# Kernel tuning notes

Hardware: AMD Instinct MI355X
Metric: run time of the kernel (lower is better)

The kernel has to match this reference:

```python
import jax, jax.numpy as jnp
import numpy as np

NUM_NODES = 10000   # nodes per graph (softmax axis)
N_HEADS = 8
IN_CHANNELS = 32
NUM_GRAPHS = 64
TOTAL_NODES = NUM_NODES * NUM_GRAPHS


def setup_inputs() -> dict:
    key = jax.random.key(0)
    k_x, k_b, k_att = jax.random.split(key, 3)
    x = jax.random.normal(k_x, (TOTAL_NODES, IN_CHANNELS), dtype=jnp.float32)
    batch = jnp.sort(jax.random.randint(k_b, (TOTAL_NODES,), 0, NUM_GRAPHS)).astype(jnp.int64)
    att = jax.random.normal(k_att, (N_HEADS, NUM_NODES), dtype=jnp.float32)
    return {"x": x, "batch": batch, "att": att, "num_graphs": NUM_GRAPHS}


def reference(x, batch, att, num_graphs):
    # x: [N, C], batch: [N], att: [H, M]; N == M * num_graphs
    B = int(num_graphs)
    w = jax.nn.softmax(att, axis=1)          # [H, M] softmax over per-graph node slots
    w_full = jnp.tile(w, (1, B))             # [H, N] tiled per graph (repeat(1,B).view(-1,1))
    # per-head weighted scatter-add pooling keyed by batch id
    pooled = jax.vmap(
        lambda wh: jax.ops.segment_sum(x * wh[:, None], batch, num_segments=B)
    )(w_full)                                # [H, B, C]
    # torch.cat(pools, dim=-1): head-major blocks along feature axis
    return pooled.transpose(1, 0, 2).reshape(B, -1)  # [B, H*C]
```

## Files before the change

### kernel.cpp

```cpp
#include <hip/hip_runtime.h>
#include <math.h>

#define H 8
#define C 32
#define HC 256
#define KSL 32
#define PB 16

__device__ __forceinline__ float wred_sum(float v) {
#pragma unroll
    for (int o = 32; o; o >>= 1) v += __shfl_xor(v, o, 64);
    return v;
}
__device__ __forceinline__ float4 red4_no(float4 v) {
#pragma unroll
    for (int o = 8; o < 64; o <<= 1) {
        v.x += __shfl_xor(v.x, o, 64);
        v.y += __shfl_xor(v.y, o, 64);
        v.z += __shfl_xor(v.z, o, 64);
        v.w += __shfl_xor(v.w, o, 64);
    }
    return v;
}

__global__ __launch_bounds__(256) void prep_kernel(
        const float* __restrict__ att, const int* __restrict__ batch,
        float* __restrict__ wtabT, int* __restrict__ segend,
        float* __restrict__ partials, int M, int Ntot, int tb, int sb) {
    const int bid = blockIdx.x;
    if (bid < tb) {
        const int idx = bid * 256 + threadIdx.x;
        if (idx < H * M) {
            const int hh = idx & (H - 1);
            const int mm = idx >> 3;
            wtabT[idx] = __expf(att[(size_t)hh * M + mm]);
        }
    } else if (bid < tb + sb) {
        const int idx = (bid - tb) * 256 + threadIdx.x;
        if (idx < Ntot) {
            const int b = batch[idx];
            if (idx == Ntot - 1 || batch[idx + 1] != b) segend[b] = idx + 1;
        }
    } else {
        const int pbid = bid - tb - sb;
        const int h = pbid / PB;
        const int p = pbid % PB;
        const int s0 = (int)(((long)M * p) / PB);
        const int s1 = (int)(((long)M * (p + 1)) / PB);
        const float* __restrict__ row = att + (size_t)h * M;
        __shared__ float red[4];
        float s = 0.f;
        for (int i = s0 + threadIdx.x; i < s1; i += 256) s += __expf(row[i]);
        s = wred_sum(s);
        if ((threadIdx.x & 63) == 0) red[threadIdx.x >> 6] = s;
        __syncthreads();
        if (threadIdx.x == 0)
            partials[h * PB + p] = red[0] + red[1] + red[2] + red[3];
    }
}

#define FMA8(XV, W0, W1)                                              \
    a0.x = fmaf(XV.x, W0.x, a0.x); a0.y = fmaf(XV.y, W0.x, a0.y);     \
    a0.z = fmaf(XV.z, W0.x, a0.z); a0.w = fmaf(XV.w, W0.x, a0.w);     \
    a1.x = fmaf(XV.x, W0.y, a1.x); a1.y = fmaf(XV.y, W0.y, a1.y);     \
    a1.z = fmaf(XV.z, W0.y, a1.z); a1.w = fmaf(XV.w, W0.y, a1.w);     \
    a2.x = fmaf(XV.x, W0.z, a2.x); a2.y = fmaf(XV.y, W0.z, a2.y);     \
    a2.z = fmaf(XV.z, W0.z, a2.z); a2.w = fmaf(XV.w, W0.z, a2.w);     \
    a3.x = fmaf(XV.x, W0.w, a3.x); a3.y = fmaf(XV.y, W0.w, a3.y);     \
    a3.z = fmaf(XV.z, W0.w, a3.z); a3.w = fmaf(XV.w, W0.w, a3.w);     \
    a4.x = fmaf(XV.x, W1.x, a4.x); a4.y = fmaf(XV.y, W1.x, a4.y);     \
    a4.z = fmaf(XV.z, W1.x, a4.z); a4.w = fmaf(XV.w, W1.x, a4.w);     \
    a5.x = fmaf(XV.x, W1.y, a5.x); a5.y = fmaf(XV.y, W1.y, a5.y);     \
    a5.z = fmaf(XV.z, W1.y, a5.z); a5.w = fmaf(XV.w, W1.y, a5.w);     \
    a6.x = fmaf(XV.x, W1.z, a6.x); a6.y = fmaf(XV.y, W1.z, a6.y);     \
    a6.z = fmaf(XV.z, W1.z, a6.z); a6.w = fmaf(XV.w, W1.z, a6.w);     \
    a7.x = fmaf(XV.x, W1.w, a7.x); a7.y = fmaf(XV.y, W1.w, a7.y);     \
    a7.z = fmaf(XV.z, W1.w, a7.z); a7.w = fmaf(XV.w, W1.w, a7.w);

__global__ __launch_bounds__(256, 5) void poolA_kernel(
        const float* __restrict__ x, const float* __restrict__ wtabT,
        const int* __restrict__ segend, float* __restrict__ psum,
        int M, int Ntot) {
    const int g  = blockIdx.x >> 5;
    const int k  = blockIdx.x & (KSL - 1);
    const int wv = threadIdx.x >> 6;
    const int lane = threadIdx.x & 63;
    const int cg = lane & 7;
    const int no = lane >> 3;
    const int c  = cg << 2;

    const int s0 = (g == 0) ? 0 : segend[g - 1];
    const int s1 = segend[g];
    const int L  = s1 - s0;
    const int sb = s0 + (int)(((long)L * k) >> 5);
    const int sl = (s0 + (int)(((long)L * (k + 1)) >> 5)) - sb;
    int       n    = sb + (sl * wv) / 4;
    const int nEnd = sb + (sl * (wv + 1)) / 4;

    float4 a0 = {0,0,0,0}, a1 = {0,0,0,0}, a2 = {0,0,0,0}, a3 = {0,0,0,0};
    float4 a4 = {0,0,0,0}, a5 = {0,0,0,0}, a6 = {0,0,0,0}, a7 = {0,0,0,0};

    int m = n % M;
    while (n < nEnd) {
        const int run = min(nEnd - n, M - m);
        const float* xb = x + (size_t)(n + no) * C + c;
        const float* wb = wtabT + ((size_t)(m + no) << 3);
        const int full = run & ~7;
        int i = 0;
#pragma unroll 2
        for (; i < full; i += 8) {
            const float4 xv  = *(const float4*)(xb + (size_t)i * C);
            const float4 wv0 = *(const float4*)(wb + (size_t)i * 8);
            const float4 wv1 = *(const float4*)(wb + (size_t)i * 8 + 4);
            FMA8(xv, wv0, wv1)
        }
        const int rem = run - full;
        if (rem) {
            const int off = (no < rem) ? no : 0;
            const float4 xv = *(const float4*)(x + (size_t)(n + i + off) * C + c);
            float4 wv0 = {0,0,0,0}, wv1 = {0,0,0,0};
            if (no < rem) {
                const float* wb2 = wtabT + ((size_t)(m + i + no) << 3);
                wv0 = *(const float4*)(wb2);
                wv1 = *(const float4*)(wb2 + 4);
            }
            FMA8(xv, wv0, wv1)
        }
        n += run;
        m += run;
        if (m >= M) m = 0;
    }

    a0 = red4_no(a0); a1 = red4_no(a1); a2 = red4_no(a2); a3 = red4_no(a3);
    a4 = red4_no(a4); a5 = red4_no(a5); a6 = red4_no(a6); a7 = red4_no(a7);

    __shared__ float4 sacc[4][H][8];
    if (no == 0) {
        sacc[wv][0][cg] = a0; sacc[wv][1][cg] = a1;
        sacc[wv][2][cg] = a2; sacc[wv][3][cg] = a3;
        sacc[wv][4][cg] = a4; sacc[wv][5][cg] = a5;
        sacc[wv][6][cg] = a6; sacc[wv][7][cg] = a7;
    }
    __syncthreads();
    if (wv == 0) {
        const int hh = lane >> 3;
        const int cc = lane & 7;
        float4 s  = sacc[0][hh][cc];
        float4 t1 = sacc[1][hh][cc];
        float4 t2 = sacc[2][hh][cc];
        float4 t3 = sacc[3][hh][cc];
        s.x += t1.x + t2.x + t3.x;
        s.y += t1.y + t2.y + t3.y;
        s.z += t1.z + t2.z + t3.z;
        s.w += t1.w + t2.w + t3.w;
        float* o = psum + ((size_t)blockIdx.x << 8) + (hh << 5) + (cc << 2);
        *(float4*)o = s;
    }
}

__global__ __launch_bounds__(256) void reduceB_kernel(
        const float* __restrict__ psum, const float* __restrict__ partials,
        float* __restrict__ out) {
    __shared__ float sinv[H];
    if (threadIdx.x < H) {
        float s = 0.f;
#pragma unroll
        for (int k = 0; k < PB; ++k) s += partials[threadIdx.x * PB + k];
        sinv[threadIdx.x] = 1.0f / s;
    }
    __syncthreads();
    const int g = blockIdx.x;
    const int i = threadIdx.x;
    const float* p = psum + ((size_t)g << 13) + i;
    float s = 0.f;
#pragma unroll
    for (int k = 0; k < KSL; ++k) s += p[(size_t)k << 8];
    out[(g << 8) + i] = s * sinv[i >> 5];
}

extern "C" void kernel_launch(void* const* d_in, const int* in_sizes, int n_in,
                              void* d_out, int out_size, void* d_ws, size_t ws_size,
                              hipStream_t stream) {
    const float* x     = (const float*)d_in[0];
    const int*   batch = (const int*)d_in[1];
    const float* att   = (const float*)d_in[2];
    float*       out   = (float*)d_out;

    const int Ntot = in_sizes[0] / C;
    const int M    = in_sizes[2] / H;
    const int B    = out_size / HC;

    float* partials = (float*)d_ws;
    int*   segend   = (int*)((char*)d_ws + 1024);
    float* wtabT    = (float*)((char*)d_ws + 4096);
    const size_t ps_off = (4096 + (size_t)H * M * sizeof(float) + 255) & ~(size_t)255;
    float* psum     = (float*)((char*)d_ws + ps_off);

    const int tb = (H * M + 255) / 256;
    const int sblocks = (Ntot + 255) / 256;
    prep_kernel<<<tb + sblocks + H * PB, 256, 0, stream>>>(
        att, batch, wtabT, segend, partials, M, Ntot, tb, sblocks);

    poolA_kernel<<<B * KSL, 256, 0, stream>>>(x, wtabT, segend, psum, M, Ntot);

    reduceB_kernel<<<B, 256, 0, stream>>>(psum, partials, out);
}
```

Baseline: 31.15 us.

## Fuse prep into pooling kernel with binary-search segments and on-the-fly exp weights

Removes the separate prep kernel. Segment boundaries are now found per block by binary search over the sorted batch array. Softmax numerators are computed inline with __expf from att using strided per-head loads instead of reading a precomputed transposed table. The softmax-denominator partial sums move into extra blocks of the pooling kernel. This saves a kernel launch and a workspace round trip, at the cost of 8 scattered loads plus 8 exps per node per lane and a log-depth search in every block.

```diff
diff --git a/kernel.cpp b/kernel.cpp
--- a/kernel.cpp
+++ b/kernel.cpp
@@ -22,41 +22,13 @@
     }
     return v;
 }
-
-__global__ __launch_bounds__(256) void prep_kernel(
-        const float* __restrict__ att, const int* __restrict__ batch,
-        float* __restrict__ wtabT, int* __restrict__ segend,
-        float* __restrict__ partials, int M, int Ntot, int tb, int sb) {
-    const int bid = blockIdx.x;
-    if (bid < tb) {
-        const int idx = bid * 256 + threadIdx.x;
-        if (idx < H * M) {
-            const int hh = idx & (H - 1);
-            const int mm = idx >> 3;
-            wtabT[idx] = __expf(att[(size_t)hh * M + mm]);
-        }
-    } else if (bid < tb + sb) {
-        const int idx = (bid - tb) * 256 + threadIdx.x;
-        if (idx < Ntot) {
-            const int b = batch[idx];
-            if (idx == Ntot - 1 || batch[idx + 1] != b) segend[b] = idx + 1;
-        }
-    } else {
-        const int pbid = bid - tb - sb;
-        const int h = pbid / PB;
-        const int p = pbid % PB;
-        const int s0 = (int)(((long)M * p) / PB);
-        const int s1 = (int)(((long)M * (p + 1)) / PB);
-        const float* __restrict__ row = att + (size_t)h * M;
-        __shared__ float red[4];
-        float s = 0.f;
-        for (int i = s0 + threadIdx.x; i < s1; i += 256) s += __expf(row[i]);
-        s = wred_sum(s);
-        if ((threadIdx.x & 63) == 0) red[threadIdx.x >> 6] = s;
-        __syncthreads();
-        if (threadIdx.x == 0)
-            partials[h * PB + p] = red[0] + red[1] + red[2] + red[3];
+__device__ __forceinline__ int lower_bound(const int* __restrict__ a, int n, int key) {
+    int lo = 0, hi = n;
+    while (lo < hi) {
+        const int mid = (lo + hi) >> 1;
+        if (a[mid] < key) lo = mid + 1; else hi = mid;
     }
+    return lo;
 }
 
 #define FMA8(XV, W0, W1)                                              \
@@ -77,20 +49,48 @@
     a7.x = fmaf(XV.x, W1.w, a7.x); a7.y = fmaf(XV.y, W1.w, a7.y);     \
     a7.z = fmaf(XV.z, W1.w, a7.z); a7.w = fmaf(XV.w, W1.w, a7.w);
 
+#define WLOAD8(MM, W0, W1)                                            \
+    { const float* ar = att + (MM);                                   \
+      W0.x = __expf(ar[0]);            W0.y = __expf(ar[M]);          \
+      W0.z = __expf(ar[2 * M]);        W0.w = __expf(ar[3 * M]);      \
+      W1.x = __expf(ar[4 * M]);        W1.y = __expf(ar[5 * M]);      \
+      W1.z = __expf(ar[6 * M]);        W1.w = __expf(ar[7 * M]); }
+
 __global__ __launch_bounds__(256, 5) void poolA_kernel(
-        const float* __restrict__ x, const float* __restrict__ wtabT,
-        const int* __restrict__ segend, float* __restrict__ psum,
-        int M, int Ntot) {
-    const int g  = blockIdx.x >> 5;
-    const int k  = blockIdx.x & (KSL - 1);
+        const float* __restrict__ x, const int* __restrict__ batch,
+        const float* __restrict__ att, float* __restrict__ psum,
+        float* __restrict__ partials, int M, int Ntot, int B) {
+    const int bid = blockIdx.x;
+    const int npool = B * KSL;
+
+    if (bid >= npool) {
+        const int pbid = bid - npool;
+        const int h = pbid / PB;
+        const int p = pbid % PB;
+        const int s0 = (int)(((long)M * p) / PB);
+        const int s1 = (int)(((long)M * (p + 1)) / PB);
+        const float* __restrict__ row = att + (size_t)h * M;
+        __shared__ float red[4];
+        float s = 0.f;
+        for (int i = s0 + threadIdx.x; i < s1; i += 256) s += __expf(row[i]);
+        s = wred_sum(s);
+        if ((threadIdx.x & 63) == 0) red[threadIdx.x >> 6] = s;
+        __syncthreads();
+        if (threadIdx.x == 0)
+            partials[h * PB + p] = red[0] + red[1] + red[2] + red[3];
+        return;
+    }
+
+    const int g  = bid >> 5;
+    const int k  = bid & (KSL - 1);
     const int wv = threadIdx.x >> 6;
     const int lane = threadIdx.x & 63;
     const int cg = lane & 7;
     const int no = lane >> 3;
     const int c  = cg << 2;
 
-    const int s0 = (g == 0) ? 0 : segend[g - 1];
-    const int s1 = segend[g];
+    const int s0 = lower_bound(batch, Ntot, g);
+    const int s1 = lower_bound(batch, Ntot, g + 1);
     const int L  = s1 - s0;
     const int sb = s0 + (int)(((long)L * k) >> 5);
     const int sl = (s0 + (int)(((long)L * (k + 1)) >> 5)) - sb;
@@ -104,14 +104,13 @@
     while (n < nEnd) {
         const int run = min(nEnd - n, M - m);
         const float* xb = x + (size_t)(n + no) * C + c;
-        const float* wb = wtabT + ((size_t)(m + no) << 3);
         const int full = run & ~7;
         int i = 0;
 #pragma unroll 2
         for (; i < full; i += 8) {
-            const float4 xv  = *(const float4*)(xb + (size_t)i * C);
-            const float4 wv0 = *(const float4*)(wb + (size_t)i * 8);
-            const float4 wv1 = *(const float4*)(wb + (size_t)i * 8 + 4);
+            const float4 xv = *(const float4*)(xb + (size_t)i * C);
+            float4 wv0, wv1;
+            WLOAD8(m + i + no, wv0, wv1)
             FMA8(xv, wv0, wv1)
         }
         const int rem = run - full;
@@ -119,11 +118,7 @@
             const int off = (no < rem) ? no : 0;
             const float4 xv = *(const float4*)(x + (size_t)(n + i + off) * C + c);
             float4 wv0 = {0,0,0,0}, wv1 = {0,0,0,0};
-            if (no < rem) {
-                const float* wb2 = wtabT + ((size_t)(m + i + no) << 3);
-                wv0 = *(const float4*)(wb2);
-                wv1 = *(const float4*)(wb2 + 4);
-            }
+            if (no < rem) { WLOAD8(m + i + no, wv0, wv1) }
             FMA8(xv, wv0, wv1)
         }
         n += run;
@@ -153,7 +148,7 @@
         s.y += t1.y + t2.y + t3.y;
         s.z += t1.z + t2.z + t3.z;
         s.w += t1.w + t2.w + t3.w;
-        float* o = psum + ((size_t)blockIdx.x << 8) + (hh << 5) + (cc << 2);
+        float* o = psum + ((size_t)bid << 8) + (hh << 5) + (cc << 2);
         *(float4*)o = s;
     }
 }
@@ -191,17 +186,10 @@
     const int B    = out_size / HC;
 
     float* partials = (float*)d_ws;
-    int*   segend   = (int*)((char*)d_ws + 1024);
-    float* wtabT    = (float*)((char*)d_ws + 4096);
-    const size_t ps_off = (4096 + (size_t)H * M * sizeof(float) + 255) & ~(size_t)255;
-    float* psum     = (float*)((char*)d_ws + ps_off);
+    float* psum     = (float*)((char*)d_ws + 4096);
 
-    const int tb = (H * M + 255) / 256;
-    const int sblocks = (Ntot + 255) / 256;
-    prep_kernel<<<tb + sblocks + H * PB, 256, 0, stream>>>(
-        att, batch, wtabT, segend, partials, M, Ntot, tb, sblocks);
-
-    poolA_kernel<<<B * KSL, 256, 0, stream>>>(x, wtabT, segend, psum, M, Ntot);
+    poolA_kernel<<<B * KSL + H * PB, 256, 0, stream>>>(
+        x, batch, att, psum, partials, M, Ntot, B);
 
     reduceB_kernel<<<B, 256, 0, stream>>>(psum, partials, out);
 }
```

New measurement: 44.29 us. 42.2% more time.
